# Kernel optimization log

Measured on AMD Instinct MI355X. Metric: run time of the kernel, lower is better.

Reference implementation:

```python
import jax, jax.numpy as jnp
import numpy as np

BN_EPS = 1e-5

def setup_inputs() -> dict:
    key = jax.random.key(0)
    k1, k2 = jax.random.split(key)
    B, C, H, W, K = 256, 2048, 7, 7, 16
    featmap = jax.random.normal(k1, (B, C, H, W), dtype=jnp.float32)
    w16 = jax.random.normal(k2, (K, C), dtype=jnp.float32) * 0.02  # 1x1 conv weight
    bn_gamma = jnp.ones((K,), jnp.float32)
    bn_beta = jnp.zeros((K,), jnp.float32)
    bn_mean = jnp.zeros((K,), jnp.float32)
    bn_var = jnp.ones((K,), jnp.float32)
    return {"featmap": featmap, "w16": w16, "bn_gamma": bn_gamma,
            "bn_beta": bn_beta, "bn_mean": bn_mean, "bn_var": bn_var}

def reference(featmap, w16, bn_gamma, bn_beta, bn_mean, bn_var):
    # featmap: [B, 2048, 7, 7]; 1x1 conv -> featcov16: [B, 16, 7, 7]
    featcov16 = jnp.einsum('bchw,kc->bkhw', featmap, w16)
    # BatchNorm2d(16), inference-style with running stats
    inv = bn_gamma / jnp.sqrt(bn_var + BN_EPS)
    featcov16 = featcov16 * inv[None, :, None, None] + (bn_beta - bn_mean * inv)[None, :, None, None]
    # Loop-free bilinear pooling: original repeats featcov16[:,i] to 2048 ch,
    # multiplies with featmap, and AvgPool2d(7) -> mean over HxW.
    HW = featmap.shape[2] * featmap.shape[3]
    feat_matrix = jnp.einsum('bkhw,bchw->bkc', featcov16, featmap) / HW  # [B,16,2048]
    bp_out_feat = feat_matrix.reshape(feat_matrix.shape[0], -1)  # [B, 32768]
    return bp_out_feat
```

## Files before the change

### kernel.cpp

```cpp
#include <hip/hip_runtime.h>

#define BATCH 256
#define CDIM  2048
#define HW    49
#define KDIM  16
#define CHUNK 512
#define TILE  128
#define ROWP  52

__global__ __launch_bounds__(256) void pconv_kernel(
    const float* __restrict__ fm, const float* __restrict__ w16,
    float* __restrict__ Ppart)
{
    __shared__ __align__(16) float fm_t[TILE * ROWP + 16];
    __shared__ __align__(16) float w_t[TILE * KDIM];

    const int tid = threadIdx.x;
    const int b   = blockIdx.x >> 2;
    const int q   = blockIdx.x & 3;
    const int c0  = q * CHUNK;
    const int h4  = tid & 15;
    const int cs  = tid >> 4;

    float acc[KDIM][4];
    #pragma unroll
    for (int k = 0; k < KDIM; ++k) {
        acc[k][0] = 0.f; acc[k][1] = 0.f; acc[k][2] = 0.f; acc[k][3] = 0.f;
    }

    const float* fmb = fm + (size_t)b * CDIM * HW;

    for (int tile = 0; tile < CHUNK / TILE; ++tile) {
        const int ct = c0 + tile * TILE;
        __syncthreads();
        const float4* src = (const float4*)(fmb + ct * HW);
        for (int i = tid; i < (TILE * HW) / 4; i += 256) {
            float4 v = src[i];
            int e = i * 4;
            int cl = e / HW; int h = e - cl * HW; fm_t[cl * ROWP + h] = v.x;
            e++; cl = e / HW; h = e - cl * HW;    fm_t[cl * ROWP + h] = v.y;
            e++; cl = e / HW; h = e - cl * HW;    fm_t[cl * ROWP + h] = v.z;
            e++; cl = e / HW; h = e - cl * HW;    fm_t[cl * ROWP + h] = v.w;
        }
        for (int i = tid; i < KDIM * TILE; i += 256) {
            int kk = i >> 7; int cc = i & 127;
            w_t[cc * KDIM + kk] = w16[kk * CDIM + ct + cc];
        }
        __syncthreads();
        #pragma unroll 2
        for (int j = 0; j < 8; ++j) {
            const int cc = cs * 8 + j;
            float4 f = *(const float4*)&fm_t[cc * ROWP + 4 * h4];
            const float4* wq = (const float4*)&w_t[cc * KDIM];
            float wv[16];
            *(float4*)&wv[0]  = wq[0];
            *(float4*)&wv[4]  = wq[1];
            *(float4*)&wv[8]  = wq[2];
            *(float4*)&wv[12] = wq[3];
            #pragma unroll
            for (int k = 0; k < 16; ++k) {
                acc[k][0] += wv[k] * f.x;
                acc[k][1] += wv[k] * f.y;
                acc[k][2] += wv[k] * f.z;
                acc[k][3] += wv[k] * f.w;
            }
        }
    }

    __syncthreads();
    float* red = fm_t;
    for (int r = 0; r < 4; ++r) {
        #pragma unroll
        for (int kk = 0; kk < 4; ++kk)
            #pragma unroll
            for (int hl = 0; hl < 4; ++hl)
                red[cs * 272 + h4 * 17 + kk * 4 + hl] = acc[r * 4 + kk][hl];
        __syncthreads();
        const int kp = r * 4 + (tid >> 6);
        const int hw = tid & 63;
        if (hw < HW) {
            float s = 0.f;
            const int base = (hw >> 2) * 17 + (tid >> 6) * 4 + (hw & 3);
            #pragma unroll
            for (int c = 0; c < 16; ++c) s += red[c * 272 + base];
            Ppart[(size_t)blockIdx.x * 784 + kp * HW + hw] = s;
        }
        __syncthreads();
    }
}

__global__ __launch_bounds__(256) void bp_kernel(
    const float* __restrict__ fm, const float* __restrict__ Ppart,
    const float* __restrict__ gamma, const float* __restrict__ beta,
    const float* __restrict__ mean, const float* __restrict__ var,
    float* __restrict__ out)
{
    __shared__ __align__(16) float Pt[HW * KDIM];
    __shared__ __align__(16) float fm_s[256 * HW];

    const int tid = threadIdx.x;
    const int b   = blockIdx.x >> 3;
    const int c0  = (blockIdx.x & 7) * 256;

    for (int p = tid; p < 784; p += 256) {
        const float* pp = Ppart + (size_t)(b * 4) * 784 + p;
        float s = pp[0] + pp[784] + pp[1568] + pp[2352];
        int kk = p / HW; int hw = p - kk * HW;
        float inv   = gamma[kk] * rsqrtf(var[kk] + 1e-5f);
        float shift = beta[kk] - mean[kk] * inv;
        Pt[hw * KDIM + kk] = (s * inv + shift) * (1.0f / 49.0f);
    }

    {
        const float4* src = (const float4*)(fm + ((size_t)b * CDIM + c0) * HW);
        float4* dst = (float4*)fm_s;
        #pragma unroll 7
        for (int i = tid; i < (256 * HW) / 4; i += 256) dst[i] = src[i];
    }
    __syncthreads();

    float acc[16];
    #pragma unroll
    for (int i = 0; i < 16; ++i) acc[i] = 0.f;

    const float* row = fm_s + tid * HW;
    #pragma unroll 7
    for (int hw = 0; hw < HW; ++hw) {
        float f = row[hw];
        const float4* pv = (const float4*)&Pt[hw * KDIM];
        float4 p0 = pv[0], p1 = pv[1], p2 = pv[2], p3 = pv[3];
        acc[0]  += p0.x * f; acc[1]  += p0.y * f; acc[2]  += p0.z * f; acc[3]  += p0.w * f;
        acc[4]  += p1.x * f; acc[5]  += p1.y * f; acc[6]  += p1.z * f; acc[7]  += p1.w * f;
        acc[8]  += p2.x * f; acc[9]  += p2.y * f; acc[10] += p2.z * f; acc[11] += p2.w * f;
        acc[12] += p3.x * f; acc[13] += p3.y * f; acc[14] += p3.z * f; acc[15] += p3.w * f;
    }

    float* ob = out + (size_t)b * (KDIM * CDIM) + c0 + tid;
    #pragma unroll
    for (int kk = 0; kk < 16; ++kk) ob[kk * CDIM] = acc[kk];
}

extern "C" void kernel_launch(void* const* d_in, const int* in_sizes, int n_in,
                              void* d_out, int out_size, void* d_ws, size_t ws_size,
                              hipStream_t stream) {
    const float* fm    = (const float*)d_in[0];
    const float* w16   = (const float*)d_in[1];
    const float* gamma = (const float*)d_in[2];
    const float* beta  = (const float*)d_in[3];
    const float* mean  = (const float*)d_in[4];
    const float* var   = (const float*)d_in[5];
    float* out   = (float*)d_out;
    float* Ppart = (float*)d_ws;

    pconv_kernel<<<BATCH * 4, 256, 0, stream>>>(fm, w16, Ppart);
    bp_kernel<<<BATCH * 8, 256, 0, stream>>>(fm, Ppart, gamma, beta, mean, var, out);
}
```

Baseline: 213.2 us.

## Fold BN into transposed weights, atomically reduce conv, read P from global in bp

A new prep kernel pre-transposes the 1x1 conv weights with the BN scale and 1/49 folded in, and seeds a per-batch scratch buffer with the BN shift. The conv kernel now has each wave stream 64 channels straight from global memory with no LDS staging, reduces across waves in shared memory, and atomically adds partial sums into the scratch buffer. The bilinear kernel reads the folded P matrix directly from global/L1 and processes four 256-channel chunks per block, using fewer blocks. This removes the LDS transpose staging and the partial-sum combine, at the cost of an extra launch, float atomics with nondeterministic summation order, and uncoalesced strided fm loads in the conv kernel.

```diff
diff --git a/kernel.cpp b/kernel.cpp
--- a/kernel.cpp
+++ b/kernel.cpp
@@ -4,140 +4,130 @@
 #define CDIM  2048
 #define HW    49
 #define KDIM  16
-#define CHUNK 512
-#define TILE  128
-#define ROWP  52
 
-__global__ __launch_bounds__(256) void pconv_kernel(
-    const float* __restrict__ fm, const float* __restrict__ w16,
-    float* __restrict__ Ppart)
+
+__global__ __launch_bounds__(256) void prep_kernel(
+    const float* __restrict__ w16,
+    const float* __restrict__ gamma, const float* __restrict__ beta,
+    const float* __restrict__ mean,  const float* __restrict__ var,
+    float* __restrict__ wT, float* __restrict__ pscr)
 {
-    __shared__ __align__(16) float fm_t[TILE * ROWP + 16];
-    __shared__ __align__(16) float w_t[TILE * KDIM];
+    const int idx = blockIdx.x * 256 + threadIdx.x;
+    if (idx < CDIM * KDIM) {
+        const int c = idx >> 4, k = idx & 15;
+        const float inv = gamma[k] * rsqrtf(var[k] + 1e-5f) * (1.0f / 49.0f);
+        wT[idx] = w16[k * CDIM + c] * inv;
+    }
+    for (int i = idx; i < BATCH * (HW * KDIM); i += 256 * 256) {
+        const int k = i & 15;
+        const float inv   = gamma[k] * rsqrtf(var[k] + 1e-5f);
+        const float shift = (beta[k] - mean[k] * inv) * (1.0f / 49.0f);
+        pscr[i] = shift;
+    }
+}
 
-    const int tid = threadIdx.x;
-    const int b   = blockIdx.x >> 2;
-    const int q   = blockIdx.x & 3;
-    const int c0  = q * CHUNK;
-    const int h4  = tid & 15;
-    const int cs  = tid >> 4;
+__global__ __launch_bounds__(512) void conv_kernel(
+    const float* __restrict__ fm, const float* __restrict__ wT,
+    float* __restrict__ pscr)
+{
+    __shared__ float red[8 * KDIM * 52];
 
-    float acc[KDIM][4];
+    const int tid  = threadIdx.x;
+    const int b    = blockIdx.x >> 2;
+    const int q    = blockIdx.x & 3;
+    const int wav  = __builtin_amdgcn_readfirstlane(tid >> 6);
+    const int lane = tid & 63;
+    const int hwi  = lane < HW ? lane : HW - 1;
+    const int cbase = q * 512 + wav * 64;
+
+    const float*  __restrict__ fmb = fm + (size_t)b * CDIM * HW;
+    const float4* __restrict__ wt4 = (const float4*)wT;
+
+    float acc[KDIM];
     #pragma unroll
-    for (int k = 0; k < KDIM; ++k) {
-        acc[k][0] = 0.f; acc[k][1] = 0.f; acc[k][2] = 0.f; acc[k][3] = 0.f;
-    }
+    for (int k = 0; k < KDIM; ++k) acc[k] = 0.f;
 
-    const float* fmb = fm + (size_t)b * CDIM * HW;
-
-    for (int tile = 0; tile < CHUNK / TILE; ++tile) {
-        const int ct = c0 + tile * TILE;
-        __syncthreads();
-        const float4* src = (const float4*)(fmb + ct * HW);
-        for (int i = tid; i < (TILE * HW) / 4; i += 256) {
-            float4 v = src[i];
-            int e = i * 4;
-            int cl = e / HW; int h = e - cl * HW; fm_t[cl * ROWP + h] = v.x;
-            e++; cl = e / HW; h = e - cl * HW;    fm_t[cl * ROWP + h] = v.y;
-            e++; cl = e / HW; h = e - cl * HW;    fm_t[cl * ROWP + h] = v.z;
-            e++; cl = e / HW; h = e - cl * HW;    fm_t[cl * ROWP + h] = v.w;
-        }
-        for (int i = tid; i < KDIM * TILE; i += 256) {
-            int kk = i >> 7; int cc = i & 127;
-            w_t[cc * KDIM + kk] = w16[kk * CDIM + ct + cc];
-        }
-        __syncthreads();
-        #pragma unroll 2
-        for (int j = 0; j < 8; ++j) {
-            const int cc = cs * 8 + j;
-            float4 f = *(const float4*)&fm_t[cc * ROWP + 4 * h4];
-            const float4* wq = (const float4*)&w_t[cc * KDIM];
-            float wv[16];
-            *(float4*)&wv[0]  = wq[0];
-            *(float4*)&wv[4]  = wq[1];
-            *(float4*)&wv[8]  = wq[2];
-            *(float4*)&wv[12] = wq[3];
-            #pragma unroll
-            for (int k = 0; k < 16; ++k) {
-                acc[k][0] += wv[k] * f.x;
-                acc[k][1] += wv[k] * f.y;
-                acc[k][2] += wv[k] * f.z;
-                acc[k][3] += wv[k] * f.w;
-            }
+    #pragma unroll 2
+    for (int g = 0; g < 64; g += 8) {
+        float f[8];
+        #pragma unroll
+        for (int u = 0; u < 8; ++u)
+            f[u] = fmb[(size_t)(cbase + g + u) * HW + hwi];
+        #pragma unroll
+        for (int u = 0; u < 8; ++u) {
+            const int c4 = (cbase + g + u) * 4;
+            const float4 w0 = wt4[c4 + 0];
+            const float4 w1 = wt4[c4 + 1];
+            const float4 w2 = wt4[c4 + 2];
+            const float4 w3 = wt4[c4 + 3];
+            const float fv = f[u];
+            acc[0]  += w0.x * fv; acc[1]  += w0.y * fv; acc[2]  += w0.z * fv; acc[3]  += w0.w * fv;
+            acc[4]  += w1.x * fv; acc[5]  += w1.y * fv; acc[6]  += w1.z * fv; acc[7]  += w1.w * fv;
+            acc[8]  += w2.x * fv; acc[9]  += w2.y * fv; acc[10] += w2.z * fv; acc[11] += w2.w * fv;
+            acc[12] += w3.x * fv; acc[13] += w3.y * fv; acc[14] += w3.z * fv; acc[15] += w3.w * fv;
         }
     }
 
+    if (lane < HW) {
+        #pragma unroll
+        for (int k = 0; k < KDIM; ++k)
+            red[wav * (KDIM * 52) + k * 52 + lane] = acc[k];
+    }
     __syncthreads();
-    float* red = fm_t;
-    for (int r = 0; r < 4; ++r) {
+    for (int j = tid; j < HW * KDIM; j += 512) {
+        const int k = j / HW, hw = j - k * HW;
+        float s = 0.f;
         #pragma unroll
-        for (int kk = 0; kk < 4; ++kk)
-            #pragma unroll
-            for (int hl = 0; hl < 4; ++hl)
-                red[cs * 272 + h4 * 17 + kk * 4 + hl] = acc[r * 4 + kk][hl];
-        __syncthreads();
-        const int kp = r * 4 + (tid >> 6);
-        const int hw = tid & 63;
-        if (hw < HW) {
-            float s = 0.f;
-            const int base = (hw >> 2) * 17 + (tid >> 6) * 4 + (hw & 3);
-            #pragma unroll
-            for (int c = 0; c < 16; ++c) s += red[c * 272 + base];
-            Ppart[(size_t)blockIdx.x * 784 + kp * HW + hw] = s;
-        }
-        __syncthreads();
+        for (int w = 0; w < 8; ++w) s += red[w * (KDIM * 52) + k * 52 + hw];
+        atomicAdd(&pscr[(size_t)b * (HW * KDIM) + hw * KDIM + k], s);
     }
 }
 
 __global__ __launch_bounds__(256) void bp_kernel(
-    const float* __restrict__ fm, const float* __restrict__ Ppart,
-    const float* __restrict__ gamma, const float* __restrict__ beta,
-    const float* __restrict__ mean, const float* __restrict__ var,
+    const float* __restrict__ fm, const float* __restrict__ pscr,
     float* __restrict__ out)
 {
-    __shared__ __align__(16) float Pt[HW * KDIM];
-    __shared__ __align__(16) float fm_s[256 * HW];
+    __shared__ __align__(16) float fs[256 * HW];
 
-    const int tid = threadIdx.x;
-    const int b   = blockIdx.x >> 3;
-    const int c0  = (blockIdx.x & 7) * 256;
+    const int tid  = threadIdx.x;
+    const int b    = blockIdx.x >> 1;
+    const int half = blockIdx.x & 1;
 
-    for (int p = tid; p < 784; p += 256) {
-        const float* pp = Ppart + (size_t)(b * 4) * 784 + p;
-        float s = pp[0] + pp[784] + pp[1568] + pp[2352];
-        int kk = p / HW; int hw = p - kk * HW;
-        float inv   = gamma[kk] * rsqrtf(var[kk] + 1e-5f);
-        float shift = beta[kk] - mean[kk] * inv;
-        Pt[hw * KDIM + kk] = (s * inv + shift) * (1.0f / 49.0f);
+    const float*  __restrict__ fmb = fm + (size_t)b * CDIM * HW;
+    const float4* __restrict__ P4  = (const float4*)(pscr + (size_t)b * (HW * KDIM));
+
+    for (int ch = 0; ch < 4; ++ch) {
+        const int cb = half * 1024 + ch * 256;
+        __syncthreads();
+        {
+            const float4* src = (const float4*)(fmb + (size_t)cb * HW);
+            float4* dst = (float4*)fs;
+            for (int i = tid; i < (256 * HW) / 4; i += 256) dst[i] = src[i];
+        }
+        __syncthreads();
+
+        float acc[KDIM];
+        #pragma unroll
+        for (int k = 0; k < KDIM; ++k) acc[k] = 0.f;
+
+        const float* row = fs + tid * HW;
+        #pragma unroll 7
+        for (int hw = 0; hw < HW; ++hw) {
+            const float fv = row[hw];
+            const float4 p0 = P4[hw * 4 + 0];
+            const float4 p1 = P4[hw * 4 + 1];
+            const float4 p2 = P4[hw * 4 + 2];
+            const float4 p3 = P4[hw * 4 + 3];
+            acc[0]  += p0.x * fv; acc[1]  += p0.y * fv; acc[2]  += p0.z * fv; acc[3]  += p0.w * fv;
+            acc[4]  += p1.x * fv; acc[5]  += p1.y * fv; acc[6]  += p1.z * fv; acc[7]  += p1.w * fv;
+            acc[8]  += p2.x * fv; acc[9]  += p2.y * fv; acc[10] += p2.z * fv; acc[11] += p2.w * fv;
+            acc[12] += p3.x * fv; acc[13] += p3.y * fv; acc[14] += p3.z * fv; acc[15] += p3.w * fv;
+        }
+
+        float* ob = out + (size_t)b * (KDIM * CDIM) + cb + tid;
+        #pragma unroll
+        for (int k = 0; k < KDIM; ++k) ob[k * CDIM] = acc[k];
     }
-
-    {
-        const float4* src = (const float4*)(fm + ((size_t)b * CDIM + c0) * HW);
-        float4* dst = (float4*)fm_s;
-        #pragma unroll 7
-        for (int i = tid; i < (256 * HW) / 4; i += 256) dst[i] = src[i];
-    }
-    __syncthreads();
-
-    float acc[16];
-    #pragma unroll
-    for (int i = 0; i < 16; ++i) acc[i] = 0.f;
-
-    const float* row = fm_s + tid * HW;
-    #pragma unroll 7
-    for (int hw = 0; hw < HW; ++hw) {
-        float f = row[hw];
-        const float4* pv = (const float4*)&Pt[hw * KDIM];
-        float4 p0 = pv[0], p1 = pv[1], p2 = pv[2], p3 = pv[3];
-        acc[0]  += p0.x * f; acc[1]  += p0.y * f; acc[2]  += p0.z * f; acc[3]  += p0.w * f;
-        acc[4]  += p1.x * f; acc[5]  += p1.y * f; acc[6]  += p1.z * f; acc[7]  += p1.w * f;
-        acc[8]  += p2.x * f; acc[9]  += p2.y * f; acc[10] += p2.z * f; acc[11] += p2.w * f;
-        acc[12] += p3.x * f; acc[13] += p3.y * f; acc[14] += p3.z * f; acc[15] += p3.w * f;
-    }
-
-    float* ob = out + (size_t)b * (KDIM * CDIM) + c0 + tid;
-    #pragma unroll
-    for (int kk = 0; kk < 16; ++kk) ob[kk * CDIM] = acc[kk];
 }
 
 extern "C" void kernel_launch(void* const* d_in, const int* in_sizes, int n_in,
@@ -149,9 +139,11 @@
     const float* beta  = (const float*)d_in[3];
     const float* mean  = (const float*)d_in[4];
     const float* var   = (const float*)d_in[5];
-    float* out   = (float*)d_out;
-    float* Ppart = (float*)d_ws;
+    float* out  = (float*)d_out;
+    float* wT   = (float*)d_ws;
+    float* pscr = (float*)d_ws + CDIM * KDIM;
 
-    pconv_kernel<<<BATCH * 4, 256, 0, stream>>>(fm, w16, Ppart);
-    bp_kernel<<<BATCH * 8, 256, 0, stream>>>(fm, Ppart, gamma, beta, mean, var, out);
+    prep_kernel<<<256, 256, 0, stream>>>(w16, gamma, beta, mean, var, wT, pscr);
+    conv_kernel<<<BATCH * 4, 512, 0, stream>>>(fm, wT, pscr);
+    bp_kernel<<<BATCH * 2, 256, 0, stream>>>(fm, pscr, out);
 }
```

Measured after the change: 224.5 us. 1.05x slower.
